# Performance work log

Measured on AMD Instinct MI355X. Metric: run time of the kernel, lower is better.

Reference implementation:

```python
import jax, jax.numpy as jnp
import numpy as np

B, T, D, H, L = 8192, 80, 32, 64, 3


def setup_inputs() -> dict:
    key = jax.random.key(0)
    ks = jax.random.split(key, 16)
    s = lambda k, shape, fan: jax.random.normal(k, shape, jnp.float32) / np.sqrt(fan)
    inp = {"x": jax.random.normal(ks[0], (B, T, D), jnp.float32)}
    dims_in = [D, H, H]
    i = 1
    for l in range(L):
        din = dims_in[l]
        inp[f"W_ih{l}"] = s(ks[i], (H, din), H); i += 1
        inp[f"W_hh{l}"] = s(ks[i], (H, H), H); i += 1
        inp[f"b_ih{l}"] = s(ks[i], (H,), H); i += 1
        inp[f"b_hh{l}"] = s(ks[i], (H,), H); i += 1
    inp["W_fc"] = s(ks[i], (1, H), H); i += 1
    inp["b_fc"] = s(ks[i], (1,), H)
    return inp


def _rnn_layer(xs, W_ih, W_hh, b_ih, b_hh):
    # xs: [T, B, Din] -> ys: [T, B, H]; tanh RNN recurrence (PyTorch nn.RNN math)
    pre = jnp.einsum('tbd,hd->tbh', xs, W_ih) + b_ih + b_hh  # input proj precomputed
    h0 = jnp.zeros((xs.shape[1], W_hh.shape[0]), xs.dtype)
    def step(h, p):
        h_new = jnp.tanh(p + h @ W_hh.T)
        return h_new, h_new
    _, ys = jax.lax.scan(step, h0, pre)
    return ys


def reference(x, W_ih0, W_hh0, b_ih0, b_hh0, W_ih1, W_hh1, b_ih1, b_hh1,
              W_ih2, W_hh2, b_ih2, b_hh2, W_fc, b_fc):
    # x: [B, T, D] (batch_first) -> time-major [T, B, D]
    h = jnp.swapaxes(x, 0, 1)
    params = [(W_ih0, W_hh0, b_ih0, b_hh0),
              (W_ih1, W_hh1, b_ih1, b_hh1),
              (W_ih2, W_hh2, b_ih2, b_hh2)]
    for (W_ih, W_hh, b_ih, b_hh) in params:
        h = _rnn_layer(h, W_ih, W_hh, b_ih, b_hh)
    last = h[-1]                      # [B, H] == out[:, -1, :]
    return last @ W_fc.T + b_fc       # [B, 1]
```

## Files before the change

kernel.cpp:

```cpp
#include <hip/hip_runtime.h>
#include <hip/hip_bf16.h>
#include <cstddef>


typedef __attribute__((ext_vector_type(8))) short s16x8;
typedef __attribute__((ext_vector_type(4))) short s16x4;
typedef __attribute__((ext_vector_type(4))) float fx4;

#define MFMA16(A, B, C) __builtin_amdgcn_mfma_f32_16x16x32_bf16((A), (B), (C), 0, 0, 0)

#if __has_builtin(__builtin_amdgcn_exp2f)
#define EXP2F(x) __builtin_amdgcn_exp2f(x)
#else
#define EXP2F(x) exp2f(x)
#endif
#if __has_builtin(__builtin_amdgcn_rcpf)
#define RCPF(x) __builtin_amdgcn_rcpf(x)
#else
#define RCPF(x) (1.0f / (x))
#endif

static constexpr float K2LOG2E = 2.8853900817779268f;

__device__ __forceinline__ short f2bf(float f) {
  union { float f; unsigned u; } v; v.f = f;
  unsigned r = v.u + 0x7FFFu + ((v.u >> 16) & 1u);
  return (short)(r >> 16);
}
__device__ __forceinline__ unsigned pk2bf(float a, float b) {
  float2 t; t.x = a; t.y = b;
  union { __hip_bfloat162 h; unsigned u; } c;
  c.h = __float22bfloat162_rn(t);
  return c.u;
}

__device__ __forceinline__ s16x8 wfragA(const float* W, int ncols, int row, int col0) {
  const float* p = W + row * ncols + col0;
  s16x8 r;
#pragma unroll
  for (int i = 0; i < 8; ++i) r[i] = f2bf(p[i]);
  return r;
}

__global__ __launch_bounds__(192, 2) void rnn3_pipe(
    const float* __restrict__ x,
    const float* __restrict__ Wih0, const float* __restrict__ Whh0,
    const float* __restrict__ bih0, const float* __restrict__ bhh0,
    const float* __restrict__ Wih1, const float* __restrict__ Whh1,
    const float* __restrict__ bih1, const float* __restrict__ bhh1,
    const float* __restrict__ Wih2, const float* __restrict__ Whh2,
    const float* __restrict__ bih2, const float* __restrict__ bhh2,
    const float* __restrict__ Wfc, const float* __restrict__ bfc,
    float* __restrict__ out)
{
  __shared__ __align__(16) short hb[3][2][16][72];

  const int tid = threadIdx.x;
  const int wv  = tid >> 6;
  const int ln  = tid & 63;
  const int q   = ln >> 4;
  const int m15 = ln & 15;
  const int bbase = (int)blockIdx.x * 16;

  const float* Wih = (wv == 0) ? Wih0 : (wv == 1) ? Wih1 : Wih2;
  const float* Whh = (wv == 0) ? Whh0 : (wv == 1) ? Whh1 : Whh2;
  const float* bi  = (wv == 0) ? bih0 : (wv == 1) ? bih1 : bih2;
  const float* bh  = (wv == 0) ? bhh0 : (wv == 1) ? bhh1 : bhh2;
  const int kin = (wv == 0) ? 32 : 64;

  s16x8 wi0[4], wi1[4], wh0[4], wh1[4];
  const s16x8 z8 = {0, 0, 0, 0, 0, 0, 0, 0};
#pragma unroll
  for (int tile = 0; tile < 4; ++tile) {
    const int row = 16 * tile + m15;
    wi0[tile] = wfragA(Wih, kin, row, 8 * q);
    wi1[tile] = wv ? wfragA(Wih, 64, row, 32 + 8 * q) : z8;
    wh0[tile] = wfragA(Whh, 64, row, 8 * q);
    wh1[tile] = wfragA(Whh, 64, row, 32 + 8 * q);
  }

  float bsc[4][4];
#pragma unroll
  for (int tile = 0; tile < 4; ++tile)
#pragma unroll
    for (int r = 0; r < 4; ++r) {
      const int j = 16 * tile + 4 * q + r;
      bsc[tile][r] = (bi[j] + bh[j]) * K2LOG2E;
    }

  const fx4 z4 = {0.f, 0.f, 0.f, 0.f};
  s16x8 r0 = z8, r1 = z8;

  const float* xr = x + (size_t)(bbase + m15) * (80 * 32) + 8 * q;
  fx4 xc0 = {0,0,0,0}, xc1 = {0,0,0,0};
  if (wv == 0) { xc0 = *(const fx4*)(xr); xc1 = *(const fx4*)(xr + 4); }

  float hk[4][4];

  for (int tau = 0; tau < 82; ++tau) {
    const int lt = tau - wv;
    if (0 <= lt && lt < 80) {
      const int p = lt & 1;
      s16x8 in0, in1;
      if (wv) {
        const short* up = &hb[wv - 1][p][m15][8 * q];
        in0 = *(const s16x8*)(up);
        in1 = *(const s16x8*)(up + 32);
      } else {
        union { unsigned u[4]; s16x8 v; } xp;
        xp.u[0] = pk2bf(xc0[0], xc0[1]); xp.u[1] = pk2bf(xc0[2], xc0[3]);
        xp.u[2] = pk2bf(xc1[0], xc1[1]); xp.u[3] = pk2bf(xc1[2], xc1[3]);
        in0 = xp.v; in1 = z8;
        const int tn = (lt < 79) ? lt + 1 : 79;
        xc0 = *(const fx4*)(xr + tn * 32);
        xc1 = *(const fx4*)(xr + tn * 32 + 4);
      }
      fx4 acc[4];
#pragma unroll
      for (int tile = 0; tile < 4; ++tile) acc[tile] = MFMA16(wh0[tile], r0, z4);
#pragma unroll
      for (int tile = 0; tile < 4; ++tile) acc[tile] = MFMA16(wh1[tile], r1, acc[tile]);
#pragma unroll
      for (int tile = 0; tile < 4; ++tile) acc[tile] = MFMA16(wi0[tile], in0, acc[tile]);
      if (wv) {
#pragma unroll
        for (int tile = 0; tile < 4; ++tile) acc[tile] = MFMA16(wi1[tile], in1, acc[tile]);
      }
      short* wb = &hb[wv][p][m15][4 * q];
#pragma unroll
      for (int tile = 0; tile < 4; ++tile) {
        float h[4];
#pragma unroll
        for (int r = 0; r < 4; ++r) {
          float e = EXP2F(__builtin_fmaf(acc[tile][r], K2LOG2E, bsc[tile][r]));
          h[r] = __builtin_fmaf(-2.f, RCPF(e + 1.f), 1.f);
          hk[tile][r] = h[r];
        }
        union { unsigned u[2]; s16x4 v; } pk;
        pk.u[0] = pk2bf(h[0], h[1]);
        pk.u[1] = pk2bf(h[2], h[3]);
        *(s16x4*)(wb + 16 * tile) = pk.v;
      }
      const short* ow = &hb[wv][p][m15][8 * q];
      r0 = *(const s16x8*)(ow);
      r1 = *(const s16x8*)(ow + 32);
    }
    __syncthreads();
  }

  if (wv == 2) {
    float s = 0.f;
#pragma unroll
    for (int tile = 0; tile < 4; ++tile)
#pragma unroll
      for (int r = 0; r < 4; ++r)
        s += hk[tile][r] * Wfc[16 * tile + 4 * q + r];
    s += __shfl_xor(s, 16, 64);
    s += __shfl_xor(s, 32, 64);
    if (ln < 16) out[bbase + ln] = s + bfc[0];
  }
}

extern "C" void kernel_launch(void* const* d_in, const int* in_sizes, int n_in,
                              void* d_out, int out_size, void* d_ws, size_t ws_size,
                              hipStream_t stream) {
  const float* x    = (const float*)d_in[0];
  const float* Wih0 = (const float*)d_in[1];
  const float* Whh0 = (const float*)d_in[2];
  const float* bih0 = (const float*)d_in[3];
  const float* bhh0 = (const float*)d_in[4];
  const float* Wih1 = (const float*)d_in[5];
  const float* Whh1 = (const float*)d_in[6];
  const float* bih1 = (const float*)d_in[7];
  const float* bhh1 = (const float*)d_in[8];
  const float* Wih2 = (const float*)d_in[9];
  const float* Whh2 = (const float*)d_in[10];
  const float* bih2 = (const float*)d_in[11];
  const float* bhh2 = (const float*)d_in[12];
  const float* Wfc  = (const float*)d_in[13];
  const float* bfc  = (const float*)d_in[14];

  rnn3_pipe<<<dim3(512), dim3(192), 0, stream>>>(
      x, Wih0, Whh0, bih0, bhh0, Wih1, Whh1, bih1, bhh1,
      Wih2, Whh2, bih2, bhh2, Wfc, bfc, (float*)d_out);
}
```

Measured before the change: 196.2 us.

## Split each RNN layer's hidden units across two wavefronts per block

Each layer's 64 hidden units are now computed by two wavefronts of 32 units each, so the block grows from 192 to 384 threads. Each wave reads its own half of the previous hidden state plus the partner half through shared memory, which halves the MFMA and tanh work per wave per timestep. The aim is to shorten the serial per-step critical path and raise the number of waves per CU. In exchange the waves exchange more through shared memory, and the final FC now reads the bf16-rounded hidden state from shared memory instead of fp32 registers.

```diff
diff --git a/kernel.cpp b/kernel.cpp
--- a/kernel.cpp
+++ b/kernel.cpp
@@ -27,6 +27,10 @@
   unsigned r = v.u + 0x7FFFu + ((v.u >> 16) & 1u);
   return (short)(r >> 16);
 }
+__device__ __forceinline__ float bf2f(short s) {
+  union { unsigned u; float f; } v; v.u = ((unsigned)(unsigned short)s) << 16;
+  return v.f;
+}
 __device__ __forceinline__ unsigned pk2bf(float a, float b) {
   float2 t; t.x = a; t.y = b;
   union { __hip_bfloat162 h; unsigned u; } c;
@@ -42,7 +46,7 @@
   return r;
 }
 
-__global__ __launch_bounds__(192, 2) void rnn3_pipe(
+__global__ __launch_bounds__(384, 3) void rnn3_pipe6(
     const float* __restrict__ x,
     const float* __restrict__ Wih0, const float* __restrict__ Whh0,
     const float* __restrict__ bih0, const float* __restrict__ bhh0,
@@ -56,108 +60,117 @@
   __shared__ __align__(16) short hb[3][2][16][72];
 
   const int tid = threadIdx.x;
-  const int wv  = tid >> 6;
+  const int wvu = __builtin_amdgcn_readfirstlane(tid >> 6);
+  const int l   = wvu >> 1;
+  const int s   = wvu & 1;
   const int ln  = tid & 63;
   const int q   = ln >> 4;
   const int m15 = ln & 15;
   const int bbase = (int)blockIdx.x * 16;
 
-  const float* Wih = (wv == 0) ? Wih0 : (wv == 1) ? Wih1 : Wih2;
-  const float* Whh = (wv == 0) ? Whh0 : (wv == 1) ? Whh1 : Whh2;
-  const float* bi  = (wv == 0) ? bih0 : (wv == 1) ? bih1 : bih2;
-  const float* bh  = (wv == 0) ? bhh0 : (wv == 1) ? bhh1 : bhh2;
-  const int kin = (wv == 0) ? 32 : 64;
+  const float* Wih = (l == 0) ? Wih0 : (l == 1) ? Wih1 : Wih2;
+  const float* Whh = (l == 0) ? Whh0 : (l == 1) ? Whh1 : Whh2;
+  const float* bi  = (l == 0) ? bih0 : (l == 1) ? bih1 : bih2;
+  const float* bh  = (l == 0) ? bhh0 : (l == 1) ? bhh1 : bhh2;
+  const int kin = (l == 0) ? 32 : 64;
 
-  s16x8 wi0[4], wi1[4], wh0[4], wh1[4];
   const s16x8 z8 = {0, 0, 0, 0, 0, 0, 0, 0};
+  s16x8 wi0[2], wi1[2], whOwn[2], whOth[2];
 #pragma unroll
-  for (int tile = 0; tile < 4; ++tile) {
-    const int row = 16 * tile + m15;
-    wi0[tile] = wfragA(Wih, kin, row, 8 * q);
-    wi1[tile] = wv ? wfragA(Wih, 64, row, 32 + 8 * q) : z8;
-    wh0[tile] = wfragA(Whh, 64, row, 8 * q);
-    wh1[tile] = wfragA(Whh, 64, row, 32 + 8 * q);
+  for (int tile = 0; tile < 2; ++tile) {
+    const int row = 32 * s + 16 * tile + m15;
+    wi0[tile]   = wfragA(Wih, kin, row, 8 * q);
+    wi1[tile]   = l ? wfragA(Wih, 64, row, 32 + 8 * q) : z8;
+    whOwn[tile] = wfragA(Whh, 64, row, 32 * s + 8 * q);
+    whOth[tile] = wfragA(Whh, 64, row, 32 * (1 - s) + 8 * q);
   }
 
-  float bsc[4][4];
+  float bsc[2][4];
 #pragma unroll
-  for (int tile = 0; tile < 4; ++tile)
+  for (int tile = 0; tile < 2; ++tile)
 #pragma unroll
     for (int r = 0; r < 4; ++r) {
-      const int j = 16 * tile + 4 * q + r;
+      const int j = 32 * s + 16 * tile + 4 * q + r;
       bsc[tile][r] = (bi[j] + bh[j]) * K2LOG2E;
     }
 
-  const fx4 z4 = {0.f, 0.f, 0.f, 0.f};
-  s16x8 r0 = z8, r1 = z8;
+  short*       wr_[2]  = {&hb[l][0][m15][32 * s + 4 * q], &hb[l][1][m15][32 * s + 4 * q]};
+  const short* own_[2] = {&hb[l][0][m15][32 * s + 8 * q], &hb[l][1][m15][32 * s + 8 * q]};
+  const short* oth_[2] = {&hb[l][0][m15][32 * (1 - s) + 8 * q],
+                          &hb[l][1][m15][32 * (1 - s) + 8 * q]};
+  const int lup = (l == 0) ? 0 : l - 1;
+  const short* up_[2]  = {&hb[lup][0][m15][8 * q], &hb[lup][1][m15][8 * q]};
 
   const float* xr = x + (size_t)(bbase + m15) * (80 * 32) + 8 * q;
-  fx4 xc0 = {0,0,0,0}, xc1 = {0,0,0,0};
-  if (wv == 0) { xc0 = *(const fx4*)(xr); xc1 = *(const fx4*)(xr + 4); }
+  fx4 xc0 = {0, 0, 0, 0}, xc1 = {0, 0, 0, 0};
+  if (l == 0) { xc0 = *(const fx4*)(xr); xc1 = *(const fx4*)(xr + 4); }
 
-  float hk[4][4];
+  const fx4 z4 = {0.f, 0.f, 0.f, 0.f};
+  s16x8 rOwn = z8;
 
   for (int tau = 0; tau < 82; ++tau) {
-    const int lt = tau - wv;
+    const int lt = tau - l;
     if (0 <= lt && lt < 80) {
-      const int p = lt & 1;
-      s16x8 in0, in1;
-      if (wv) {
-        const short* up = &hb[wv - 1][p][m15][8 * q];
-        in0 = *(const s16x8*)(up);
-        in1 = *(const s16x8*)(up + 32);
-      } else {
+      const int p  = lt & 1;
+      const int pm = p ^ 1;
+      s16x8 rOth = z8;
+      if (lt > 0) rOth = *(const s16x8*)(oth_[pm]);
+      s16x8 in0, in1 = z8;
+      if (l == 0) {
         union { unsigned u[4]; s16x8 v; } xp;
         xp.u[0] = pk2bf(xc0[0], xc0[1]); xp.u[1] = pk2bf(xc0[2], xc0[3]);
         xp.u[2] = pk2bf(xc1[0], xc1[1]); xp.u[3] = pk2bf(xc1[2], xc1[3]);
-        in0 = xp.v; in1 = z8;
+        in0 = xp.v;
         const int tn = (lt < 79) ? lt + 1 : 79;
         xc0 = *(const fx4*)(xr + tn * 32);
         xc1 = *(const fx4*)(xr + tn * 32 + 4);
+      } else {
+        const short* up = up_[p];
+        in0 = *(const s16x8*)(up);
+        in1 = *(const s16x8*)(up + 32);
       }
-      fx4 acc[4];
+      fx4 acc[2];
 #pragma unroll
-      for (int tile = 0; tile < 4; ++tile) acc[tile] = MFMA16(wh0[tile], r0, z4);
+      for (int tile = 0; tile < 2; ++tile) acc[tile] = MFMA16(whOwn[tile], rOwn, z4);
 #pragma unroll
-      for (int tile = 0; tile < 4; ++tile) acc[tile] = MFMA16(wh1[tile], r1, acc[tile]);
+      for (int tile = 0; tile < 2; ++tile) acc[tile] = MFMA16(whOth[tile], rOth, acc[tile]);
 #pragma unroll
-      for (int tile = 0; tile < 4; ++tile) acc[tile] = MFMA16(wi0[tile], in0, acc[tile]);
-      if (wv) {
+      for (int tile = 0; tile < 2; ++tile) acc[tile] = MFMA16(wi0[tile], in0, acc[tile]);
+      if (l) {
 #pragma unroll
-        for (int tile = 0; tile < 4; ++tile) acc[tile] = MFMA16(wi1[tile], in1, acc[tile]);
+        for (int tile = 0; tile < 2; ++tile) acc[tile] = MFMA16(wi1[tile], in1, acc[tile]);
       }
-      short* wb = &hb[wv][p][m15][4 * q];
+      short* wb = wr_[p];
 #pragma unroll
-      for (int tile = 0; tile < 4; ++tile) {
+      for (int tile = 0; tile < 2; ++tile) {
         float h[4];
 #pragma unroll
         for (int r = 0; r < 4; ++r) {
           float e = EXP2F(__builtin_fmaf(acc[tile][r], K2LOG2E, bsc[tile][r]));
           h[r] = __builtin_fmaf(-2.f, RCPF(e + 1.f), 1.f);
-          hk[tile][r] = h[r];
         }
         union { unsigned u[2]; s16x4 v; } pk;
         pk.u[0] = pk2bf(h[0], h[1]);
         pk.u[1] = pk2bf(h[2], h[3]);
         *(s16x4*)(wb + 16 * tile) = pk.v;
       }
-      const short* ow = &hb[wv][p][m15][8 * q];
-      r0 = *(const s16x8*)(ow);
-      r1 = *(const s16x8*)(ow + 32);
+      rOwn = *(const s16x8*)(own_[p]);
     }
     __syncthreads();
   }
 
-  if (wv == 2) {
-    float s = 0.f;
+  if (wvu == 4) {
+    const short* f = &hb[2][1][m15][8 * q];
+    s16x8 f0 = *(const s16x8*)(f);
+    s16x8 f1 = *(const s16x8*)(f + 32);
+    float sv = 0.f;
 #pragma unroll
-    for (int tile = 0; tile < 4; ++tile)
+    for (int i = 0; i < 8; ++i) sv += bf2f(f0[i]) * Wfc[8 * q + i];
 #pragma unroll
-      for (int r = 0; r < 4; ++r)
-        s += hk[tile][r] * Wfc[16 * tile + 4 * q + r];
-    s += __shfl_xor(s, 16, 64);
-    s += __shfl_xor(s, 32, 64);
-    if (ln < 16) out[bbase + ln] = s + bfc[0];
+    for (int i = 0; i < 8; ++i) sv += bf2f(f1[i]) * Wfc[32 + 8 * q + i];
+    sv += __shfl_xor(sv, 16, 64);
+    sv += __shfl_xor(sv, 32, 64);
+    if (ln < 16) out[bbase + ln] = sv + bfc[0];
   }
 }
 
@@ -180,7 +193,7 @@
   const float* Wfc  = (const float*)d_in[13];
   const float* bfc  = (const float*)d_in[14];
 
-  rnn3_pipe<<<dim3(512), dim3(192), 0, stream>>>(
+  rnn3_pipe6<<<dim3(512), dim3(384), 0, stream>>>(
       x, Wih0, Whh0, bih0, bhh0, Wih1, Whh1, bih1, bhh1,
       Wih2, Whh2, bih2, bhh2, Wfc, bfc, (float*)d_out);
 }
```

Result: slower. 209.0 us (+6.5%).
